# Kernel optimization log

Measured on AMD Instinct MI355X. Metric: run time of the kernel, lower is better.

Reference implementation:

```python
import jax, jax.numpy as jnp
import numpy as np

LOG2 = float(np.log(2.0))

def _ssp(x):
    # shifted softplus: ln(0.5*(exp(x)+1)) = softplus(x) - ln 2
    return jax.nn.softplus(x) - LOG2

def setup_inputs() -> dict:
    key = jax.random.key(0)
    ks = jax.random.split(key, 8)
    B, N, D = 32, 512, 1024
    H = D // 2
    s = lambda fan_in: 1.0 / np.sqrt(fan_in)
    return {
        "representation": jax.random.normal(ks[0], (B, N, D), jnp.float32),
        "R": jax.random.normal(ks[1], (B, N, 3), jnp.float32),
        "atom_mask": jnp.ones((B, N), jnp.float32),
        "W1": jax.random.normal(ks[2], (D, H), jnp.float32) * s(D),
        "b1": jnp.zeros((H,), jnp.float32),
        "W2": jax.random.normal(ks[3], (H, 1), jnp.float32) * s(H),
        "b2": jnp.zeros((1,), jnp.float32),
        "Wc1": jax.random.normal(ks[4], (D, H), jnp.float32) * s(D),
        "bc1": jnp.zeros((H,), jnp.float32),
        "Wc2": jax.random.normal(ks[5], (H, 1), jnp.float32) * s(H),
        "bc2": jnp.zeros((1,), jnp.float32),
    }

def reference(representation, R, atom_mask, W1, b1, W2, b2, Wc1, bc1, Wc2, bc2):
    B, N, _ = representation.shape
    # Atomwise pyramidal MLP: n_in -> n_in//2 (shifted softplus) -> 1
    yi = _ssp(jnp.einsum("bnd,dh->bnh", representation, W1) + b1)
    yi = jnp.einsum("bnh,ho->bno", yi, W2) + b2            # [B,N,1]
    # masked sum pool over atoms (mean=0, stddev=1 so standardize is identity)
    y = jnp.sum(yi * atom_mask[..., None], axis=1)          # [B,1]

    # pairwise distances with safe sqrt (diag is exactly zero)
    diff = R[:, None, :, :] - R[:, :, None, :]              # [B,N,N,3]
    d2 = jnp.sum(diff * diff, axis=-1)                      # [B,N,N]
    dist = jnp.where(d2 > 0, jnp.sqrt(jnp.where(d2 > 0, d2, 1.0)), 0.0)

    eye = jnp.eye(N, dtype=dist.dtype)
    tot_mask = atom_mask[:, None, :] * atom_mask[:, :, None] * (1.0 - eye)
    keep = (tot_mask != 0).astype(dist.dtype)               # [B,N,N]
    dist = dist * keep

    # charge net: Dense(n_in, n_in//2, ssp) -> Dense(n_in//2, 1)
    q = _ssp(jnp.einsum("bnd,dh->bnh", representation, Wc1) + bc1)
    q = jnp.einsum("bnh,ho->bno", q, Wc2) + bc2             # [B,N,1]

    inv2 = (1e-5 + dist) ** -2                              # [B,N,N]
    coulomb = q[:, :, 0][:, None, :] * inv2 * q             # [B,N,N] (q_j * inv * q_i)
    coulomb = coulomb * keep
    e = jnp.sum(coulomb, axis=(1, 2))                       # [B]

    return y + e[:, None]                                   # [B,1]
```

## Files before the change

### kernel.cpp

```cpp
#include <hip/hip_runtime.h>
#include <math.h>


typedef unsigned short u16;
typedef unsigned int u32;
typedef __bf16 bf16x8 __attribute__((ext_vector_type(8)));
typedef float f32x4 __attribute__((ext_vector_type(4)));

#define GK 1024
#define NT 16

#define GLOAD_LDS16(g, l) __builtin_amdgcn_global_load_lds( \
    (const __attribute__((address_space(1))) void*)(g),     \
    (__attribute__((address_space(3))) void*)(l), 16, 0, 0)

__device__ __forceinline__ u16 f2bf(float f) {
    u32 u = __float_as_uint(f);
    return (u16)((u + 0x7FFFu + ((u >> 16) & 1u)) >> 16);
}

__device__ __forceinline__ float ssp_f(float x) {
    return __logf(0.5f * (__expf(x) + 1.0f));
}

__device__ __forceinline__ float ssp_slow(float x) {
    return fmaxf(x, 0.0f) + log1pf(expf(-fabsf(x))) - 0.6931471805599453f;
}


__global__ __launch_bounds__(256) void prep(
    const float* __restrict__ rep, const float* __restrict__ W1,
    const float* __restrict__ Wc1, u16* __restrict__ Abf,
    u16* __restrict__ Bp, float* __restrict__ out)
{
    __shared__ float tile[32][33];
    const int blk = blockIdx.x;
    const int t = threadIdx.x;
    if (blk < 8192) {
        int i = (blk * 256 + t) * 8;
        float4 x = *(const float4*)(rep + i);
        float4 y = *(const float4*)(rep + i + 4);
        union { u16 h[8]; uint4 v; } o;
        o.h[0] = f2bf(x.x); o.h[1] = f2bf(x.y); o.h[2] = f2bf(x.z); o.h[3] = f2bf(x.w);
        o.h[4] = f2bf(y.x); o.h[5] = f2bf(y.y); o.h[6] = f2bf(y.z); o.h[7] = f2bf(y.w);
        *(uint4*)(Abf + i) = o.v;
        if (blk == 0 && t < 32) out[t] = 0.0f;
    } else {
        const int bb = blk - 8192;
        const int k0 = (bb & 31) * 32;
        const int n0 = (bb >> 5) * 32;
        const float* src = (n0 < 512) ? W1 : Wc1;
        const int ns0 = (n0 < 512) ? n0 : n0 - 512;
#pragma unroll
        for (int j = 0; j < 4; j++) {
            int idx = j * 256 + t;
            int kl = idx >> 5, nl = idx & 31;
            tile[kl][nl] = src[(size_t)(k0 + kl) * 512 + ns0 + nl];
        }
        __syncthreads();
#pragma unroll
        for (int j = 0; j < 4; j++) {
            int idx = j * 256 + t;
            int nl = idx >> 5, kl = idx & 31;
            int n = n0 + nl;
            int c16 = n >> 4, lmv = n & 15;
            int kt32 = k0 >> 5, qv = kl >> 3, jv = kl & 7;
            Bp[(size_t)(((c16 * 32 + kt32) * 64) + qv * 16 + lmv) * 8 + jv] =
                f2bf(tile[kl][nl]);
        }
    }
}


__global__ __launch_bounds__(512, 2) void gemm_mfma(
    const u16* __restrict__ A,
    const u16* __restrict__ Bp,
    const float* __restrict__ b1, const float* __restrict__ W2,
    const float* __restrict__ bc1, const float* __restrict__ Wc2,
    float* __restrict__ parts)
{
    __shared__ u16 smem[3][16384];

    const int blk = blockIdx.x;
    const int swz = ((blk & 7) << 5) | (blk >> 3);
    const int bm = swz >> 2;
    const int bn = swz & 3;
    const int tid = threadIdx.x;
    const int w = tid >> 6, lane = tid & 63;
    const int wm = w & 1, wn = w >> 1;
    const int lm = lane & 15, q = lane >> 4;

    f32x4 acc[8][4];
#pragma unroll
    for (int i = 0; i < 8; i++)
#pragma unroll
        for (int j = 0; j < 4; j++)
            acc[i][j] = (f32x4){0.0f, 0.0f, 0.0f, 0.0f};

    int goff[2][2];
#pragma unroll
    for (int h = 0; h < 2; h++)
#pragma unroll
        for (int p2 = 0; p2 < 2; p2++) {
            int ci = h * 1024 + (w * 2 + p2) * 64 + lane;
            int row = ci >> 3;
            int c = (ci & 7) ^ (row & 7);
            goff[h][p2] = row * GK + c * 8;
        }

    int arow[4], aswz[2];
#pragma unroll
    for (int mi = 0; mi < 4; mi++) arow[mi] = (wm * 128 + mi * 16 + lm) * 64;
#pragma unroll
    for (int kk = 0; kk < 2; kk++) aswz[kk] = ((kk * 4 + q) ^ (lm & 7)) * 8;

    const u16* Ab = A + (size_t)bm * 256 * GK;
    const u16* Bw = Bp + (size_t)(bn * 16 + wn * 4) * 16384 + lane * 8;

#define STAGE_A3(SB, TN) do {                                                 \
    const u16* gA_ = Ab + (TN) * 64;                                          \
    GLOAD_LDS16(gA_ + goff[0][0], (SB) + ((w * 2 + 0) * 64) * 8);             \
    GLOAD_LDS16(gA_ + goff[0][1], (SB) + ((w * 2 + 1) * 64) * 8);             \
    GLOAD_LDS16(gA_ + goff[1][0], (SB) + (1024 + (w * 2 + 0) * 64) * 8);      \
    GLOAD_LDS16(gA_ + goff[1][1], (SB) + (1024 + (w * 2 + 1) * 64) * 8);      \
} while (0)

#define LOAD_B(DST, T)                                                        \
    _Pragma("unroll") for (int nj = 0; nj < 4; nj++)                          \
    _Pragma("unroll") for (int kk = 0; kk < 2; kk++)                          \
        DST[nj][kk] = *(const bf16x8*)&Bw[nj * 16384 + ((T) * 2 + kk) * 512];

#define READ_A(SB, MH, DST)                                                   \
    _Pragma("unroll") for (int mi = 0; mi < 4; mi++)                          \
    _Pragma("unroll") for (int kk = 0; kk < 2; kk++)                          \
        DST[mi][kk] = *(const bf16x8*)&(SB)[arow[mi] + (MH) * 4096 + aswz[kk]];

#define MFMA_HALF(MH, AF, BF)                                                 \
    _Pragma("unroll") for (int kk = 0; kk < 2; kk++)                          \
    _Pragma("unroll") for (int mi = 0; mi < 4; mi++)                          \
    _Pragma("unroll") for (int nj = 0; nj < 4; nj++)                          \
        acc[(MH) * 4 + mi][nj] = __builtin_amdgcn_mfma_f32_16x16x32_bf16(     \
            AF[mi][kk], BF[nj][kk], acc[(MH) * 4 + mi][nj], 0, 0, 0);

    bf16x8 afrX[4][2], afrY[4][2], bf[4][2];

    STAGE_A3(&smem[0][0], 0);
    STAGE_A3(&smem[1][0], 1);
    asm volatile("s_waitcnt vmcnt(0)" ::: "memory");
    __builtin_amdgcn_sched_barrier(0);
    __builtin_amdgcn_s_barrier();
    __builtin_amdgcn_sched_barrier(0);

    for (int t = 0; t < NT; ++t) {
        u16* sC = &smem[t % 3][0];
        u16* sN = &smem[(t + 2) % 3][0];

        LOAD_B(bf, t);
        if (t < NT - 2) STAGE_A3(sN, t + 2);

        READ_A(sC, 0, afrX);
        READ_A(sC, 1, afrY);

        __builtin_amdgcn_s_setprio(1);
        MFMA_HALF(0, afrX, bf);
        MFMA_HALF(1, afrY, bf);
        __builtin_amdgcn_s_setprio(0);

        __builtin_amdgcn_sched_barrier(0);
        __builtin_amdgcn_s_barrier();
        __builtin_amdgcn_sched_barrier(0);
    }

#undef STAGE_A3
#undef LOAD_B
#undef READ_A
#undef MFMA_HALF

    asm volatile("s_waitcnt vmcnt(0)" ::: "memory");
    __syncthreads();
    float* red = (float*)&smem[0][0];
    const bool is_q = (bn >= 2);
    const float* bb2 = is_q ? bc1 : b1;
    const float* vv = is_q ? Wc2 : W2;
    float bias[4], v[4];
#pragma unroll
    for (int nfr = 0; nfr < 4; nfr++) {
        int c = (bn & 1) * 256 + wn * 64 + nfr * 16 + lm;
        bias[nfr] = bb2[c];
        v[nfr] = vv[c];
    }
#pragma unroll
    for (int mfr = 0; mfr < 8; mfr++) {
#pragma unroll
        for (int r = 0; r < 4; r++) {
            float s = 0.0f;
#pragma unroll
            for (int nfr = 0; nfr < 4; nfr++)
                s += v[nfr] * ssp_f(acc[mfr][nfr][r] + bias[nfr]);
            s += __shfl_xor(s, 1);
            s += __shfl_xor(s, 2);
            s += __shfl_xor(s, 4);
            s += __shfl_xor(s, 8);
            if (lm == 0) red[wn * 256 + wm * 128 + mfr * 16 + q * 4 + r] = s;
        }
    }
    __syncthreads();
    if (tid < 256) {
        float val = red[0 * 256 + tid] + red[1 * 256 + tid] +
                    red[2 * 256 + tid] + red[3 * 256 + tid];
        parts[(size_t)bn * 16384 + bm * 256 + tid] = val;
    }
}


__global__ __launch_bounds__(256) void coulomb_k(
    const float* __restrict__ R, const float* __restrict__ mask,
    const float* __restrict__ parts, const float* __restrict__ b2p,
    const float* __restrict__ bc2p, float* __restrict__ out)
{
    const int N = 512;
    const int b = blockIdx.y;
    const int chunk = blockIdx.x;
    __shared__ float Rx[512], Ry[512], Rz[512], QM[512];
    __shared__ float rbuf[4];
    const int tid = threadIdx.x;
    const float bc2 = bc2p[0];
    const float b2 = b2p[0];

    for (int j = tid; j < N; j += 256) {
        int idx = b * N + j;
        float m = mask[idx];
        const float* rp = R + (size_t)idx * 3;
        Rx[j] = rp[0];
        Ry[j] = rp[1];
        Rz[j] = rp[2];
        float qv = parts[2 * 16384 + idx] + parts[3 * 16384 + idx] + bc2;
        QM[j] = qv * m;
    }
    __syncthreads();

    const int i = chunk * 64 + (tid & 63);
    const int js = (tid >> 6) * 128;
    const float xi = Rx[i], yi = Ry[i], zi = Rz[i], qmi = QM[i];
    float e = 0.0f;
    for (int j = js; j < js + 128; j++) {
        float dx = xi - Rx[j];
        float dy = yi - Ry[j];
        float dz = zi - Rz[j];
        float d2 = dx * dx + dy * dy + dz * dz;
        float t = 1e-5f + sqrtf(d2);
        float term = qmi * QM[j] / (t * t);
        e += (j == i) ? 0.0f : term;
    }
    if (tid < 64) {
        int ii = b * N + chunk * 64 + tid;
        float yv = parts[0 * 16384 + ii] + parts[1 * 16384 + ii] + b2;
        e += yv * mask[ii];
    }
    for (int off = 32; off > 0; off >>= 1) e += __shfl_down(e, off, 64);
    if ((tid & 63) == 0) rbuf[tid >> 6] = e;
    __syncthreads();
    if (tid == 0) atomicAdd(&out[b], rbuf[0] + rbuf[1] + rbuf[2] + rbuf[3]);
}


#define BM 128
#define BN 64
#define BK 16

__global__ __launch_bounds__(256) void mlp_gemm(
    const float* __restrict__ A, const float* __restrict__ W1,
    const float* __restrict__ Wc1, const float* __restrict__ b1,
    const float* __restrict__ bc1, const float* __restrict__ W2,
    const float* __restrict__ Wc2, float* __restrict__ yi_part,
    float* __restrict__ q_part)
{
    const int K = 1024;
    const int bm = blockIdx.x;
    const int bn = blockIdx.y;
    const bool is_q = (bn >= 8);
    const float* __restrict__ W = is_q ? Wc1 : W1;
    const int j0 = (bn & 7) * BN;

    __shared__ float As[BK][BM + 4];
    __shared__ float Bs[BK][BN + 4];
    __shared__ float red[BM];

    const int tid = threadIdx.x;
    const int tx = tid & 15;
    const int ty = tid >> 4;

    float acc[8][4];
#pragma unroll
    for (int r = 0; r < 8; r++)
#pragma unroll
        for (int c = 0; c < 4; c++) acc[r][c] = 0.0f;

    const int a_row = tid >> 2;
    const int a_k4 = (tid & 3) * 4;
    const float* Arow0 = A + (size_t)(bm * BM + a_row) * K;
    const float* Arow1 = Arow0 + (size_t)64 * K;
    const int w_k = tid >> 4;
    const int w_j = (tid & 15) * 4;

    for (int kt = 0; kt < K; kt += BK) {
        float4 av0 = *(const float4*)(Arow0 + kt + a_k4);
        float4 av1 = *(const float4*)(Arow1 + kt + a_k4);
        float4 wv = *(const float4*)(W + (size_t)(kt + w_k) * 512 + j0 + w_j);
        __syncthreads();
        As[a_k4 + 0][a_row] = av0.x;
        As[a_k4 + 1][a_row] = av0.y;
        As[a_k4 + 2][a_row] = av0.z;
        As[a_k4 + 3][a_row] = av0.w;
        As[a_k4 + 0][a_row + 64] = av1.x;
        As[a_k4 + 1][a_row + 64] = av1.y;
        As[a_k4 + 2][a_row + 64] = av1.z;
        As[a_k4 + 3][a_row + 64] = av1.w;
        *(float4*)&Bs[w_k][w_j] = wv;
        __syncthreads();
#pragma unroll
        for (int kk = 0; kk < BK; kk++) {
            float4 a0 = *(const float4*)&As[kk][ty * 8];
            float4 a1 = *(const float4*)&As[kk][ty * 8 + 4];
            float4 bv = *(const float4*)&Bs[kk][tx * 4];
            float ar[8] = {a0.x, a0.y, a0.z, a0.w, a1.x, a1.y, a1.z, a1.w};
            float bc[4] = {bv.x, bv.y, bv.z, bv.w};
#pragma unroll
            for (int r = 0; r < 8; r++)
#pragma unroll
                for (int c = 0; c < 4; c++)
                    acc[r][c] = fmaf(ar[r], bc[c], acc[r][c]);
        }
    }

    const float* bb = is_q ? bc1 : b1;
    const float* vv = is_q ? Wc2 : W2;
    float bias[4], v[4];
#pragma unroll
    for (int c = 0; c < 4; c++) {
        bias[c] = bb[j0 + tx * 4 + c];
        v[c] = vv[j0 + tx * 4 + c];
    }
    if (tid < BM) red[tid] = 0.0f;
    __syncthreads();
#pragma unroll
    for (int r = 0; r < 8; r++) {
        float s = 0.0f;
#pragma unroll
        for (int c = 0; c < 4; c++)
            s += v[c] * ssp_slow(acc[r][c] + bias[c]);
        atomicAdd(&red[ty * 8 + r], s);
    }
    __syncthreads();
    float* target = is_q ? q_part : yi_part;
    if (tid < BM) atomicAdd(&target[(size_t)bm * BM + tid], red[tid]);
}

__global__ __launch_bounds__(256) void coulomb_fb(
    const float* __restrict__ R, const float* __restrict__ mask,
    const float* __restrict__ yi_part, const float* __restrict__ q_part,
    const float* __restrict__ b2p, const float* __restrict__ bc2p,
    float* __restrict__ out)
{
    const int N = 512;
    const int b = blockIdx.y;
    const int chunk = blockIdx.x;
    __shared__ float Rx[512], Ry[512], Rz[512], QM[512];
    __shared__ float rbuf[4];
    const int tid = threadIdx.x;
    const float bc2 = bc2p[0];
    const float b2 = b2p[0];

    for (int j = tid; j < N; j += 256) {
        float m = mask[b * N + j];
        const float* rp = R + ((size_t)b * N + j) * 3;
        Rx[j] = rp[0];
        Ry[j] = rp[1];
        Rz[j] = rp[2];
        QM[j] = (q_part[b * N + j] + bc2) * m;
    }
    __syncthreads();

    const int i = chunk * 64 + (tid & 63);
    const int js = (tid >> 6) * 128;
    const float xi = Rx[i], yi = Ry[i], zi = Rz[i], qmi = QM[i];
    float e = 0.0f;
    for (int j = js; j < js + 128; j++) {
        float dx = xi - Rx[j];
        float dy = yi - Ry[j];
        float dz = zi - Rz[j];
        float d2 = dx * dx + dy * dy + dz * dz;
        float t = 1e-5f + sqrtf(d2);
        float term = qmi * QM[j] / (t * t);
        e += (j == i) ? 0.0f : term;
    }
    if (tid < 64) {
        int ii = chunk * 64 + tid;
        e += (yi_part[b * N + ii] + b2) * mask[b * N + ii];
    }
    for (int off = 32; off > 0; off >>= 1) e += __shfl_down(e, off, 64);
    if ((tid & 63) == 0) rbuf[tid >> 6] = e;
    __syncthreads();
    if (tid == 0) atomicAdd(&out[b], rbuf[0] + rbuf[1] + rbuf[2] + rbuf[3]);
}


extern "C" void kernel_launch(void* const* d_in, const int* in_sizes, int n_in,
                              void* d_out, int out_size, void* d_ws, size_t ws_size,
                              hipStream_t stream) {
    const float* rep  = (const float*)d_in[0];
    const float* R    = (const float*)d_in[1];
    const float* mask = (const float*)d_in[2];
    const float* W1   = (const float*)d_in[3];
    const float* b1   = (const float*)d_in[4];
    const float* W2   = (const float*)d_in[5];
    const float* b2   = (const float*)d_in[6];
    const float* Wc1  = (const float*)d_in[7];
    const float* bc1  = (const float*)d_in[8];
    const float* Wc2  = (const float*)d_in[9];
    const float* bc2  = (const float*)d_in[10];
    float* out = (float*)d_out;

    const size_t szA = 16384ull * 1024 * 2;
    const size_t szB = 1024ull * 1024 * 2;
    const size_t szP = 8ull * 16384 * 4;
    const size_t need = szA + szB + szP;

    if (ws_size >= need) {
        u16* Abf = (u16*)d_ws;
        u16* Bpk = (u16*)((char*)d_ws + szA);
        float* parts = (float*)((char*)d_ws + szA + szB);

        prep<<<8192 + 1024, 256, 0, stream>>>(rep, W1, Wc1, Abf, Bpk, out);
        gemm_mfma<<<256, 512, 0, stream>>>(Abf, Bpk, b1, W2, bc1, Wc2, parts);
        coulomb_k<<<dim3(8, 32), 256, 0, stream>>>(R, mask, parts, b2, bc2, out);
    } else {
        float* yi_part = (float*)d_ws;
        float* q_part = yi_part + 16384;
        hipMemsetAsync(d_ws, 0, 2 * 16384 * sizeof(float), stream);
        hipMemsetAsync(d_out, 0, 32 * sizeof(float), stream);
        mlp_gemm<<<dim3(128, 16), 256, 0, stream>>>(rep, W1, Wc1, b1, bc1, W2, Wc2,
                                                    yi_part, q_part);
        coulomb_fb<<<dim3(8, 32), 256, 0, stream>>>(R, mask, yi_part, q_part, b2, bc2, out);
    }
}
```

Baseline: 171.1 us.

## Restructure MFMA GEMM mainloop to double-buffered LDS with prefetched B and inline ds_reads

Changes the A-tile pipeline from a three-stage LDS ring with two tiles in flight to a two-buffer ping-pong. The next A tile and the next B fragments are prefetched into alternate registers while the current tile computes. LDS reads become inline-asm ds_read_b128 with immediate offsets from precomputed base addresses. Each half's MFMAs start right after its own reads with explicit lgkmcnt waits, and the barrier waits with vmcnt(8) instead of draining all loads. This cuts LDS use and address arithmetic and overlaps the B global loads with compute, but shortens prefetch depth and depends on hand-set waitcnt values being correct.

```diff
diff --git a/kernel.cpp b/kernel.cpp
--- a/kernel.cpp
+++ b/kernel.cpp
@@ -79,7 +79,7 @@
     const float* __restrict__ bc1, const float* __restrict__ Wc2,
     float* __restrict__ parts)
 {
-    __shared__ u16 smem[3][16384];
+    __shared__ u16 smem[2][16384];
 
     const int blk = blockIdx.x;
     const int swz = ((blk & 7) << 5) | (blk >> 3);
@@ -108,11 +108,14 @@
             goff[h][p2] = row * GK + c * 8;
         }
 
-    int arow[4], aswz[2];
-#pragma unroll
-    for (int mi = 0; mi < 4; mi++) arow[mi] = (wm * 128 + mi * 16 + lm) * 64;
-#pragma unroll
-    for (int kk = 0; kk < 2; kk++) aswz[kk] = ((kk * 4 + q) ^ (lm & 7)) * 8;
+    const int arow0 = (wm * 128 + lm) * 64;
+    const int aswz0 = (q ^ (lm & 7)) * 8;
+    const int aswz1 = ((4 + q) ^ (lm & 7)) * 8;
+    const u32 base0 = (u32)(size_t)(__attribute__((address_space(3))) void*)&smem[0][0];
+    const u32 a0 = base0 + 2u * (u32)(arow0 + aswz0);
+    const u32 a1 = base0 + 2u * (u32)(arow0 + aswz1);
+    const u32 c0 = a0 + 32768u;
+    const u32 c1 = a1 + 32768u;
 
     const u16* Ab = A + (size_t)bm * 256 * GK;
     const u16* Bw = Bp + (size_t)(bn * 16 + wn * 4) * 16384 + lane * 8;
@@ -130,10 +133,22 @@
     _Pragma("unroll") for (int kk = 0; kk < 2; kk++)                          \
         DST[nj][kk] = *(const bf16x8*)&Bw[nj * 16384 + ((T) * 2 + kk) * 512];
 
-#define READ_A(SB, MH, DST)                                                   \
-    _Pragma("unroll") for (int mi = 0; mi < 4; mi++)                          \
-    _Pragma("unroll") for (int kk = 0; kk < 2; kk++)                          \
-        DST[mi][kk] = *(const bf16x8*)&(SB)[arow[mi] + (MH) * 4096 + aswz[kk]];
+#define DSR(D, AD, O) asm volatile("ds_read_b128 %0, %1 offset:" O          \
+                                   : "=v"(D) : "v"(AD))
+
+#define READ_HALF0(A0, A1, F) do {                                            \
+    DSR(F[0][0], A0, "0");     DSR(F[0][1], A1, "0");                         \
+    DSR(F[1][0], A0, "2048");  DSR(F[1][1], A1, "2048");                      \
+    DSR(F[2][0], A0, "4096");  DSR(F[2][1], A1, "4096");                      \
+    DSR(F[3][0], A0, "6144");  DSR(F[3][1], A1, "6144");                      \
+} while (0)
+
+#define READ_HALF1(A0, A1, F) do {                                            \
+    DSR(F[0][0], A0, "8192");  DSR(F[0][1], A1, "8192");                      \
+    DSR(F[1][0], A0, "10240"); DSR(F[1][1], A1, "10240");                     \
+    DSR(F[2][0], A0, "12288"); DSR(F[2][1], A1, "12288");                     \
+    DSR(F[3][0], A0, "14336"); DSR(F[3][1], A1, "14336");                     \
+} while (0)
 
 #define MFMA_HALF(MH, AF, BF)                                                 \
     _Pragma("unroll") for (int kk = 0; kk < 2; kk++)                          \
@@ -142,41 +157,54 @@
         acc[(MH) * 4 + mi][nj] = __builtin_amdgcn_mfma_f32_16x16x32_bf16(     \
             AF[mi][kk], BF[nj][kk], acc[(MH) * 4 + mi][nj], 0, 0, 0);
 
-    bf16x8 afrX[4][2], afrY[4][2], bf[4][2];
+#define TILE(RD0, RD1, STG, BC, BN, T) do {                                   \
+    if ((T) < NT - 1) {                                                       \
+        STAGE_A3(STG, (T) + 1);                                               \
+        LOAD_B(BN, (T) + 1);                                                  \
+    }                                                                         \
+    READ_HALF0(RD0, RD1, afrX);                                               \
+    asm volatile("s_waitcnt lgkmcnt(0)" ::: "memory");                        \
+    __builtin_amdgcn_sched_barrier(0);                                        \
+    __builtin_amdgcn_s_setprio(1);                                            \
+    MFMA_HALF(0, afrX, BC);                                                   \
+    __builtin_amdgcn_s_setprio(0);                                            \
+    READ_HALF1(RD0, RD1, afrY);                                               \
+    asm volatile("s_waitcnt lgkmcnt(0)" ::: "memory");                        \
+    __builtin_amdgcn_sched_barrier(0);                                        \
+    __builtin_amdgcn_s_setprio(1);                                            \
+    MFMA_HALF(1, afrY, BC);                                                   \
+    __builtin_amdgcn_s_setprio(0);                                            \
+    asm volatile("s_waitcnt vmcnt(8)" ::: "memory");                          \
+    __builtin_amdgcn_sched_barrier(0);                                        \
+    __builtin_amdgcn_s_barrier();                                             \
+    __builtin_amdgcn_sched_barrier(0);                                        \
+} while (0)
+
+    bf16x8 afrX[4][2], afrY[4][2], bfA[4][2], bfB[4][2];
 
     STAGE_A3(&smem[0][0], 0);
-    STAGE_A3(&smem[1][0], 1);
-    asm volatile("s_waitcnt vmcnt(0)" ::: "memory");
+    LOAD_B(bfA, 0);
+    asm volatile("s_waitcnt vmcnt(8)" ::: "memory");
     __builtin_amdgcn_sched_barrier(0);
     __builtin_amdgcn_s_barrier();
     __builtin_amdgcn_sched_barrier(0);
 
-    for (int t = 0; t < NT; ++t) {
-        u16* sC = &smem[t % 3][0];
-        u16* sN = &smem[(t + 2) % 3][0];
-
-        LOAD_B(bf, t);
-        if (t < NT - 2) STAGE_A3(sN, t + 2);
-
-        READ_A(sC, 0, afrX);
-        READ_A(sC, 1, afrY);
-
-        __builtin_amdgcn_s_setprio(1);
-        MFMA_HALF(0, afrX, bf);
-        MFMA_HALF(1, afrY, bf);
-        __builtin_amdgcn_s_setprio(0);
-
-        __builtin_amdgcn_sched_barrier(0);
-        __builtin_amdgcn_s_barrier();
-        __builtin_amdgcn_sched_barrier(0);
-    }
+    for (int tt = 0; tt < 8; ++tt) {
+        const int t0 = 2 * tt, t1 = 2 * tt + 1;
+        TILE(a0, a1, &smem[1][0], bfA, bfB, t0);
+        TILE(c0, c1, &smem[0][0], bfB, bfA, t1);
+    }
+
+    asm volatile("s_waitcnt vmcnt(0)" ::: "memory");
 
 #undef STAGE_A3
 #undef LOAD_B
-#undef READ_A
+#undef DSR
+#undef READ_HALF0
+#undef READ_HALF1
 #undef MFMA_HALF
-
-    asm volatile("s_waitcnt vmcnt(0)" ::: "memory");
+#undef TILE
+
     __syncthreads();
     float* red = (float*)&smem[0][0];
     const bool is_q = (bn >= 2);
@@ -320,10 +348,10 @@
         __syncthreads();
 #pragma unroll
         for (int kk = 0; kk < BK; kk++) {
-            float4 a0 = *(const float4*)&As[kk][ty * 8];
-            float4 a1 = *(const float4*)&As[kk][ty * 8 + 4];
+            float4 a0v = *(const float4*)&As[kk][ty * 8];
+            float4 a1v = *(const float4*)&As[kk][ty * 8 + 4];
             float4 bv = *(const float4*)&Bs[kk][tx * 4];
-            float ar[8] = {a0.x, a0.y, a0.z, a0.w, a1.x, a1.y, a1.z, a1.w};
+            float ar[8] = {a0v.x, a0v.y, a0v.z, a0v.w, a1v.x, a1v.y, a1v.z, a1v.w};
             float bc[4] = {bv.x, bv.y, bv.z, bv.w};
 #pragma unroll
             for (int r = 0; r < 8; r++)
```

Measured after the change: 171.9 us. Within noise of the previous version (+0.5%).
